# Optimization experiments

Hardware: AMD Instinct MI355X
Metric: run time of the kernel (lower is better)

Reference implementation:

```python
import jax, jax.numpy as jnp
import numpy as np

K1, K2 = 0.01, 0.03
DATA_RANGE = 1.0
EPS = 1e-6


def setup_inputs() -> dict:
    key = jax.random.key(0)
    k1, k2, k3 = jax.random.split(key, 3)
    B, C, H, W = 4, 3, 256, 176
    S, M = 5, 18
    X = jax.random.normal(k1, (B, C, H, W), dtype=jnp.float32)
    Y = jax.random.normal(k2, (B, C, H, W), dtype=jnp.float32)
    bp_mask = jax.random.uniform(k3, (B, S, M, H, W), dtype=jnp.float32)
    return {"X": X, "Y": Y, "bp_mask": bp_mask}


def reference(X, Y, bp_mask):
    # Rescale from [-1, 1] to [0, 1]
    X = (X + 1.0) / 2.0
    Y = (Y + 1.0) / 2.0
    C1 = (K1 * DATA_RANGE) ** 2
    C2 = (K2 * DATA_RANGE) ** 2

    # Normalized mask weights: [B, S, M, H, W]
    msum = bp_mask.sum(axis=(-2, -1), keepdims=True)
    w = bp_mask / (msum + EPS)

    # Masked first / second moments -> [B, S, M, C], no repeated 6D tensors
    mu1 = jnp.einsum('bchw,bsmhw->bsmc', X, w)
    mu2 = jnp.einsum('bchw,bsmhw->bsmc', Y, w)
    mu11 = jnp.einsum('bchw,bsmhw->bsmc', X * X, w)
    mu22 = jnp.einsum('bchw,bsmhw->bsmc', Y * Y, w)
    mu12 = jnp.einsum('bchw,bsmhw->bsmc', X * Y, w)

    mu1_sq = mu1 * mu1
    mu2_sq = mu2 * mu2
    mu1_mu2 = mu1 * mu2
    sigma1_sq = mu11 - mu1_sq
    sigma2_sq = mu22 - mu2_sq
    sigma12 = mu12 - mu1_mu2

    cs = (2.0 * sigma12 + C2) / (sigma1_sq + sigma2_sq + C2)
    ssim = (2.0 * mu1_mu2 + C1) / (mu1_sq + mu2_sq + C1) * cs
    # nonnegative_ssim=True
    ssim = jax.nn.relu(ssim)
    cs = jax.nn.relu(cs)

    # Mean over merged (M, C) axis -> [B, S]
    cs_batch = cs.mean(axis=(2, 3))
    ssim_batch = ssim.mean(axis=(2, 3))

    msssim = jnp.prod(cs_batch[:, :-1], axis=1) * ssim_batch[:, -1]
    return msssim.mean()
```

## Files before the change

kernel.cpp:

```cpp
#include <hip/hip_runtime.h>

#define B_  4
#define C_  3
#define S_  5
#define M_  18
#define HW  45056
#define HW4 (HW/4)
#define SPLIT 11
#define TPB 256
#define CHUNK4 (HW4/SPLIT)
#define ITERS (CHUNK4/TPB)
#define NPLANE (B_*S_*M_)

typedef float f4 __attribute__((ext_vector_type(4)));

#define ACC1(WC, XC, YC, c) do { \
    float wx = (WC) * (XC); \
    float wy = (WC) * (YC); \
    a1[c]  += wx; \
    a2[c]  += wy; \
    a11[c] = fmaf(wx, (XC), a11[c]); \
    a22[c] = fmaf(wy, (YC), a22[c]); \
    a12[c] = fmaf(wx, (YC), a12[c]); \
  } while (0)

__global__ __launch_bounds__(TPB) void moments_kernel(
    const float4* __restrict__ X, const float4* __restrict__ Y,
    const f4* __restrict__ Mk, float* __restrict__ part) {
  int bid   = blockIdx.x;
  int plane = bid / SPLIT;
  int chunk = bid - plane * SPLIT;
  int b     = plane / (S_ * M_);

  const f4*     mp = Mk + (size_t)plane * HW4;
  const float4* xp = X  + (size_t)b * (C_ * HW4);
  const float4* yp = Y  + (size_t)b * (C_ * HW4);

  int base = chunk * CHUNK4 + (int)threadIdx.x;

  float aW = 0.f;
  float a1[C_], a2[C_], a11[C_], a22[C_], a12[C_];
#pragma unroll
  for (int c = 0; c < C_; ++c) { a1[c]=a2[c]=a11[c]=a22[c]=a12[c]=0.f; }

#pragma unroll
  for (int it = 0; it < ITERS; ++it) {
    int i = base + it * TPB;
    f4 w = __builtin_nontemporal_load(mp + i);
    aW += (w.x + w.y) + (w.z + w.w);
#pragma unroll
    for (int c = 0; c < C_; ++c) {
      float4 xv = xp[c * HW4 + i];
      float4 yv = yp[c * HW4 + i];
      ACC1(w.x, xv.x, yv.x, c);
      ACC1(w.y, xv.y, yv.y, c);
      ACC1(w.z, xv.z, yv.z, c);
      ACC1(w.w, xv.w, yv.w, c);
    }
  }

  float v[16];
  v[0] = aW;
#pragma unroll
  for (int c = 0; c < C_; ++c) {
    v[1 + c*5 + 0] = a1[c];
    v[1 + c*5 + 1] = a2[c];
    v[1 + c*5 + 2] = a11[c];
    v[1 + c*5 + 3] = a22[c];
    v[1 + c*5 + 4] = a12[c];
  }

#pragma unroll
  for (int off = 32; off > 0; off >>= 1) {
#pragma unroll
    for (int j = 0; j < 16; ++j) v[j] += __shfl_xor(v[j], off);
  }

  __shared__ float red[TPB/64][16];
  int lane = threadIdx.x & 63;
  int wv   = threadIdx.x >> 6;
  if (lane == 0) {
#pragma unroll
    for (int j = 0; j < 16; ++j) red[wv][j] = v[j];
  }
  __syncthreads();
  if (threadIdx.x < 16) {
    float s = (red[0][threadIdx.x] + red[1][threadIdx.x]) +
              (red[2][threadIdx.x] + red[3][threadIdx.x]);
    part[(size_t)bid * 16 + threadIdx.x] = s;
  }
}

__global__ __launch_bounds__(384) void finalize_kernel(
    const float* __restrict__ part, float* __restrict__ out) {
  __shared__ float csS[NPLANE], ssS[NPLANE];
  __shared__ double csb[B_*S_], ssb[B_*S_];
  int t = threadIdx.x;

  if (t < NPLANE) {
    double s[16];
#pragma unroll
    for (int j = 0; j < 16; ++j) s[j] = 0.0;
    for (int ch = 0; ch < SPLIT; ++ch) {
      const float* p = part + (size_t)(t * SPLIT + ch) * 16;
#pragma unroll
      for (int j = 0; j < 16; ++j) s[j] += (double)p[j];
    }
    const double C1d = 1e-4, C2d = 9e-4;
    double W = s[0];
    double inv = 1.0 / (W + 1e-6);
    double csAcc = 0.0, ssAcc = 0.0;
#pragma unroll
    for (int c = 0; c < C_; ++c) {
      double S1  = s[1 + c*5 + 0];
      double S2  = s[1 + c*5 + 1];
      double S11 = s[1 + c*5 + 2];
      double S22 = s[1 + c*5 + 3];
      double S12 = s[1 + c*5 + 4];
      double mu1  = (0.5*S1 + 0.5*W) * inv;
      double mu2  = (0.5*S2 + 0.5*W) * inv;
      double mu11 = (0.25*S11 + 0.5*S1 + 0.25*W) * inv;
      double mu22 = (0.25*S22 + 0.5*S2 + 0.25*W) * inv;
      double mu12 = (0.25*(S12 + S1 + S2 + W)) * inv;
      double m1s = mu1*mu1, m2s = mu2*mu2, m12 = mu1*mu2;
      double sig1  = mu11 - m1s;
      double sig2  = mu22 - m2s;
      double sig12 = mu12 - m12;
      double cs   = (2.0*sig12 + C2d) / (sig1 + sig2 + C2d);
      double ssim = (2.0*m12 + C1d) / (m1s + m2s + C1d) * cs;
      if (cs   < 0.0) cs   = 0.0;
      if (ssim < 0.0) ssim = 0.0;
      csAcc += cs; ssAcc += ssim;
    }
    csS[t] = (float)csAcc;
    ssS[t] = (float)ssAcc;
  }
  __syncthreads();

  if (t < B_*S_) {
    double cb = 0.0, sb = 0.0;
    for (int m = 0; m < M_; ++m) { cb += (double)csS[t*M_ + m]; sb += (double)ssS[t*M_ + m]; }
    csb[t] = cb / (double)(M_*C_);
    ssb[t] = sb / (double)(M_*C_);
  }
  __syncthreads();

  if (t == 0) {
    double acc = 0.0;
    for (int b = 0; b < B_; ++b) {
      double p = ssb[b*S_ + (S_-1)];
      for (int s = 0; s < S_-1; ++s) p *= csb[b*S_ + s];
      acc += p;
    }
    out[0] = (float)(acc / (double)B_);
  }
}

extern "C" void kernel_launch(void* const* d_in, const int* in_sizes, int n_in,
                              void* d_out, int out_size, void* d_ws, size_t ws_size,
                              hipStream_t stream) {
  (void)in_sizes; (void)n_in; (void)out_size; (void)ws_size;
  const float4* X  = (const float4*)d_in[0];
  const float4* Y  = (const float4*)d_in[1];
  const f4*     Mk = (const f4*)d_in[2];
  float* part = (float*)d_ws;
  float* out  = (float*)d_out;

  hipLaunchKernelGGL(moments_kernel, dim3(NPLANE*SPLIT), dim3(TPB), 0, stream,
                     X, Y, Mk, part);
  hipLaunchKernelGGL(finalize_kernel, dim3(1), dim3(384), 0, stream, part, out);
}
```

Measured before the change: 127.8 us.

## Process three mask planes per block to reuse X/Y loads and precompute products

Each workgroup now handles a group of three mask planes over a larger pixel chunk, so every X/Y load and the xx, yy, xy products feed three planes instead of one. This cuts the repeated X/Y traffic and the per-pixel ALU work. Block IDs are also remapped with a stride-8 swizzle, likely to spread work across XCDs, and launch bounds now request two blocks per CU. The cost is far more accumulator registers (48 values plus three mask loads per iteration), fewer and larger blocks, and a longer shuffle reduction.

```diff
diff --git a/kernel.cpp b/kernel.cpp
--- a/kernel.cpp
+++ b/kernel.cpp
@@ -6,88 +6,114 @@
 #define M_  18
 #define HW  45056
 #define HW4 (HW/4)
-#define SPLIT 11
+#define G   3
+#define MG  (M_/G)
+#define SPLIT 4
 #define TPB 256
 #define CHUNK4 (HW4/SPLIT)
 #define ITERS (CHUNK4/TPB)
+#define NGROUP (B_*S_*MG)
+#define NBLK (NGROUP*SPLIT)
 #define NPLANE (B_*S_*M_)
 
 typedef float f4 __attribute__((ext_vector_type(4)));
 
-#define ACC1(WC, XC, YC, c) do { \
-    float wx = (WC) * (XC); \
-    float wy = (WC) * (YC); \
-    a1[c]  += wx; \
-    a2[c]  += wy; \
-    a11[c] = fmaf(wx, (XC), a11[c]); \
-    a22[c] = fmaf(wy, (YC), a22[c]); \
-    a12[c] = fmaf(wx, (YC), a12[c]); \
-  } while (0)
-
-__global__ __launch_bounds__(TPB) void moments_kernel(
+__global__ __launch_bounds__(TPB, 2) void moments_kernel(
     const float4* __restrict__ X, const float4* __restrict__ Y,
     const f4* __restrict__ Mk, float* __restrict__ part) {
-  int bid   = blockIdx.x;
-  int plane = bid / SPLIT;
-  int chunk = bid - plane * SPLIT;
-  int b     = plane / (S_ * M_);
-
-  const f4*     mp = Mk + (size_t)plane * HW4;
-  const float4* xp = X  + (size_t)b * (C_ * HW4);
-  const float4* yp = Y  + (size_t)b * (C_ * HW4);
+  int wg    = (blockIdx.x & 7) * (NBLK / 8) + (blockIdx.x >> 3);
+  int group = wg / SPLIT;
+  int chunk = wg - group * SPLIT;
+  int bs    = group / MG;
+  int mg    = group - bs * MG;
+  int b     = bs / S_;
+
+  const f4* mp0 = Mk + (size_t)(bs * M_ + mg * G + 0) * HW4;
+  const f4* mp1 = Mk + (size_t)(bs * M_ + mg * G + 1) * HW4;
+  const f4* mp2 = Mk + (size_t)(bs * M_ + mg * G + 2) * HW4;
+  const float4* xp = X + (size_t)b * (C_ * HW4);
+  const float4* yp = Y + (size_t)b * (C_ * HW4);
 
   int base = chunk * CHUNK4 + (int)threadIdx.x;
 
-  float aW = 0.f;
-  float a1[C_], a2[C_], a11[C_], a22[C_], a12[C_];
-#pragma unroll
-  for (int c = 0; c < C_; ++c) { a1[c]=a2[c]=a11[c]=a22[c]=a12[c]=0.f; }
+  float aW[G];
+  float a1[G][C_], a2[G][C_], a11[G][C_], a22[G][C_], a12[G][C_];
+#pragma unroll
+  for (int g = 0; g < G; ++g) {
+    aW[g] = 0.f;
+#pragma unroll
+    for (int c = 0; c < C_; ++c) {
+      a1[g][c]=a2[g][c]=a11[g][c]=a22[g][c]=a12[g][c]=0.f;
+    }
+  }
 
 #pragma unroll
   for (int it = 0; it < ITERS; ++it) {
     int i = base + it * TPB;
-    f4 w = __builtin_nontemporal_load(mp + i);
-    aW += (w.x + w.y) + (w.z + w.w);
+    f4 w0 = __builtin_nontemporal_load(mp0 + i);
+    f4 w1 = __builtin_nontemporal_load(mp1 + i);
+    f4 w2 = __builtin_nontemporal_load(mp2 + i);
+    float wv[G][4] = {{w0.x,w0.y,w0.z,w0.w},
+                      {w1.x,w1.y,w1.z,w1.w},
+                      {w2.x,w2.y,w2.z,w2.w}};
+    aW[0] += (w0.x + w0.y) + (w0.z + w0.w);
+    aW[1] += (w1.x + w1.y) + (w1.z + w1.w);
+    aW[2] += (w2.x + w2.y) + (w2.z + w2.w);
 #pragma unroll
     for (int c = 0; c < C_; ++c) {
       float4 xv = xp[c * HW4 + i];
       float4 yv = yp[c * HW4 + i];
-      ACC1(w.x, xv.x, yv.x, c);
-      ACC1(w.y, xv.y, yv.y, c);
-      ACC1(w.z, xv.z, yv.z, c);
-      ACC1(w.w, xv.w, yv.w, c);
-    }
-  }
-
-  float v[16];
-  v[0] = aW;
-#pragma unroll
-  for (int c = 0; c < C_; ++c) {
-    v[1 + c*5 + 0] = a1[c];
-    v[1 + c*5 + 1] = a2[c];
-    v[1 + c*5 + 2] = a11[c];
-    v[1 + c*5 + 3] = a22[c];
-    v[1 + c*5 + 4] = a12[c];
+      float xvf[4] = {xv.x, xv.y, xv.z, xv.w};
+      float yvf[4] = {yv.x, yv.y, yv.z, yv.w};
+#pragma unroll
+      for (int j = 0; j < 4; ++j) {
+        float xc = xvf[j], yc = yvf[j];
+        float xx = xc * xc, yy = yc * yc, xy = xc * yc;
+#pragma unroll
+        for (int g = 0; g < G; ++g) {
+          float wc = wv[g][j];
+          a1 [g][c] = fmaf(wc, xc, a1 [g][c]);
+          a2 [g][c] = fmaf(wc, yc, a2 [g][c]);
+          a11[g][c] = fmaf(wc, xx, a11[g][c]);
+          a22[g][c] = fmaf(wc, yy, a22[g][c]);
+          a12[g][c] = fmaf(wc, xy, a12[g][c]);
+        }
+      }
+    }
+  }
+
+  float v[G*16];
+#pragma unroll
+  for (int g = 0; g < G; ++g) {
+    v[g*16 + 0] = aW[g];
+#pragma unroll
+    for (int c = 0; c < C_; ++c) {
+      v[g*16 + 1 + c*5 + 0] = a1 [g][c];
+      v[g*16 + 1 + c*5 + 1] = a2 [g][c];
+      v[g*16 + 1 + c*5 + 2] = a11[g][c];
+      v[g*16 + 1 + c*5 + 3] = a22[g][c];
+      v[g*16 + 1 + c*5 + 4] = a12[g][c];
+    }
   }
 
 #pragma unroll
   for (int off = 32; off > 0; off >>= 1) {
 #pragma unroll
-    for (int j = 0; j < 16; ++j) v[j] += __shfl_xor(v[j], off);
-  }
-
-  __shared__ float red[TPB/64][16];
+    for (int j = 0; j < G*16; ++j) v[j] += __shfl_xor(v[j], off);
+  }
+
+  __shared__ float red[TPB/64][G*16];
   int lane = threadIdx.x & 63;
-  int wv   = threadIdx.x >> 6;
+  int wv_  = threadIdx.x >> 6;
   if (lane == 0) {
 #pragma unroll
-    for (int j = 0; j < 16; ++j) red[wv][j] = v[j];
+    for (int j = 0; j < G*16; ++j) red[wv_][j] = v[j];
   }
   __syncthreads();
-  if (threadIdx.x < 16) {
+  if (threadIdx.x < G*16) {
     float s = (red[0][threadIdx.x] + red[1][threadIdx.x]) +
               (red[2][threadIdx.x] + red[3][threadIdx.x]);
-    part[(size_t)bid * 16 + threadIdx.x] = s;
+    part[(size_t)wg * (G*16) + threadIdx.x] = s;
   }
 }
 
@@ -98,11 +124,17 @@
   int t = threadIdx.x;
 
   if (t < NPLANE) {
+    int bs = t / M_;
+    int mrem = t - bs * M_;
+    int mg = mrem / G;
+    int g  = mrem - mg * G;
+    int group = bs * MG + mg;
+
     double s[16];
 #pragma unroll
     for (int j = 0; j < 16; ++j) s[j] = 0.0;
     for (int ch = 0; ch < SPLIT; ++ch) {
-      const float* p = part + (size_t)(t * SPLIT + ch) * 16;
+      const float* p = part + ((size_t)(group * SPLIT + ch) * G + g) * 16;
 #pragma unroll
       for (int j = 0; j < 16; ++j) s[j] += (double)p[j];
     }
@@ -166,7 +198,7 @@
   float* part = (float*)d_ws;
   float* out  = (float*)d_out;
 
-  hipLaunchKernelGGL(moments_kernel, dim3(NPLANE*SPLIT), dim3(TPB), 0, stream,
+  hipLaunchKernelGGL(moments_kernel, dim3(NBLK), dim3(TPB), 0, stream,
                      X, Y, Mk, part);
   hipLaunchKernelGGL(finalize_kernel, dim3(1), dim3(384), 0, stream, part, out);
 }
```

Measured after the change: 122.9 us. 3.9% less time.

## Remap blocks across XCDs, cut split count, use plain mask loads

Applied to the files above, without the earlier changes.

Blocks are renumbered so that each group of consecutive work items lands on the same XCD. The aim is for the blocks of a plane, and the planes that share the same batch X/Y data, to reuse L2 on one die. The per-plane split drops from 11 to 4, so each thread runs more iterations and writes fewer partials. The non-temporal mask load becomes a normal cached load. Fewer blocks may reduce latency hiding and load balance across the CUs.

```diff
diff --git a/kernel.cpp b/kernel.cpp
--- a/kernel.cpp
+++ b/kernel.cpp
@@ -6,33 +6,23 @@
 #define M_  18
 #define HW  45056
 #define HW4 (HW/4)
-#define SPLIT 11
+#define SPLIT 4
 #define TPB 256
 #define CHUNK4 (HW4/SPLIT)
 #define ITERS (CHUNK4/TPB)
 #define NPLANE (B_*S_*M_)
+#define NBLK (NPLANE*SPLIT)
 
-typedef float f4 __attribute__((ext_vector_type(4)));
-
-#define ACC1(WC, XC, YC, c) do { \
-    float wx = (WC) * (XC); \
-    float wy = (WC) * (YC); \
-    a1[c]  += wx; \
-    a2[c]  += wy; \
-    a11[c] = fmaf(wx, (XC), a11[c]); \
-    a22[c] = fmaf(wy, (YC), a22[c]); \
-    a12[c] = fmaf(wx, (YC), a12[c]); \
-  } while (0)
 
 __global__ __launch_bounds__(TPB) void moments_kernel(
     const float4* __restrict__ X, const float4* __restrict__ Y,
-    const f4* __restrict__ Mk, float* __restrict__ part) {
-  int bid   = blockIdx.x;
-  int plane = bid / SPLIT;
-  int chunk = bid - plane * SPLIT;
+    const float4* __restrict__ Mk, float* __restrict__ part) {
+  int wg    = (blockIdx.x & 7) * (NBLK / 8) + (blockIdx.x >> 3);
+  int plane = wg / SPLIT;
+  int chunk = wg - plane * SPLIT;
   int b     = plane / (S_ * M_);
 
-  const f4*     mp = Mk + (size_t)plane * HW4;
+  const float4* mp = Mk + (size_t)plane * HW4;
   const float4* xp = X  + (size_t)b * (C_ * HW4);
   const float4* yp = Y  + (size_t)b * (C_ * HW4);
 
@@ -46,16 +36,26 @@
 #pragma unroll
   for (int it = 0; it < ITERS; ++it) {
     int i = base + it * TPB;
-    f4 w = __builtin_nontemporal_load(mp + i);
+    float4 w  = mp[i];
     aW += (w.x + w.y) + (w.z + w.w);
+    float wf[4] = {w.x, w.y, w.z, w.w};
 #pragma unroll
     for (int c = 0; c < C_; ++c) {
       float4 xv = xp[c * HW4 + i];
       float4 yv = yp[c * HW4 + i];
-      ACC1(w.x, xv.x, yv.x, c);
-      ACC1(w.y, xv.y, yv.y, c);
-      ACC1(w.z, xv.z, yv.z, c);
-      ACC1(w.w, xv.w, yv.w, c);
+      float xf[4] = {xv.x, xv.y, xv.z, xv.w};
+      float yf[4] = {yv.x, yv.y, yv.z, yv.w};
+#pragma unroll
+      for (int j = 0; j < 4; ++j) {
+        float xc = xf[j], yc = yf[j], wc = wf[j];
+        float wx = wc * xc;
+        float wy = wc * yc;
+        a1 [c] += wx;
+        a2 [c] += wy;
+        a11[c]  = fmaf(wx, xc, a11[c]);
+        a22[c]  = fmaf(wy, yc, a22[c]);
+        a12[c]  = fmaf(wx, yc, a12[c]);
+      }
     }
   }
 
@@ -87,7 +87,7 @@
   if (threadIdx.x < 16) {
     float s = (red[0][threadIdx.x] + red[1][threadIdx.x]) +
               (red[2][threadIdx.x] + red[3][threadIdx.x]);
-    part[(size_t)bid * 16 + threadIdx.x] = s;
+    part[(size_t)wg * 16 + threadIdx.x] = s;
   }
 }
 
@@ -162,11 +162,11 @@
   (void)in_sizes; (void)n_in; (void)out_size; (void)ws_size;
   const float4* X  = (const float4*)d_in[0];
   const float4* Y  = (const float4*)d_in[1];
-  const f4*     Mk = (const f4*)d_in[2];
+  const float4* Mk = (const float4*)d_in[2];
   float* part = (float*)d_ws;
   float* out  = (float*)d_out;
 
-  hipLaunchKernelGGL(moments_kernel, dim3(NPLANE*SPLIT), dim3(TPB), 0, stream,
+  hipLaunchKernelGGL(moments_kernel, dim3(NBLK), dim3(TPB), 0, stream,
                      X, Y, Mk, part);
   hipLaunchKernelGGL(finalize_kernel, dim3(1), dim3(384), 0, stream, part, out);
 }
```

Result: faster. 121.7 us, median of 3 (-4.8%).
